# Optimization experiments

Hardware: AMD Instinct MI355X
Metric: run time of the kernel (lower is better)

Reference implementation:

```python
import jax, jax.numpy as jnp
import numpy as np

X, Y, F, B = 128, 128, 256, 2048
SIGMA = 2.0
LR = 0.5


def setup_inputs() -> dict:
    key = jax.random.key(0)
    k1, k2 = jax.random.split(key)
    data = jax.random.normal(k1, (B, F), dtype=jnp.float32)
    # weights init per module: 2*randn - 1, then L2-normalized along features
    w = 2.0 * jax.random.normal(k2, (X, Y, F), dtype=jnp.float32) - 1.0
    w = w / jnp.linalg.norm(w, axis=-1, keepdims=True)
    return {"data": data, "weights": w}


def reference(data, weights):
    # --- BMU search: euclidean cdist from each sample to every neuron ---
    wf = weights.reshape(X * Y, F)  # [N, F]
    d2 = (
        jnp.sum(data * data, axis=-1)[:, None]
        + jnp.sum(wf * wf, axis=-1)[None, :]
        - 2.0 * data @ wf.T
    )  # [B, N]
    dist = jnp.sqrt(jnp.maximum(d2, 0.0))
    idx = jnp.argmin(dist, axis=1)  # [B]
    bmu_x = idx // Y  # row coord
    bmu_y = idx % Y   # col coord

    # --- Gaussian neighborhood on the rectangular grid, one per sample ---
    xs = jnp.arange(X, dtype=jnp.float32)
    ys = jnp.arange(Y, dtype=jnp.float32)
    dx2 = (xs[None, :] - bmu_x[:, None].astype(jnp.float32)) ** 2  # [B, X]
    dy2 = (ys[None, :] - bmu_y[:, None].astype(jnp.float32)) ** 2  # [B, Y]
    nb = jnp.exp(-(dx2[:, :, None] + dy2[:, None, :]) / (2.0 * SIGMA * SIGMA))  # [B, X, Y]

    # --- Batch weight update: mean_b lr * nb_b * (data_b - W) ---
    # Avoid materializing the [B, X, Y, F] update tensor; same math via contraction.
    weighted_data = jnp.einsum("bxy,bf->xyf", nb, data)  # sum_b nb*data
    nb_sum = jnp.sum(nb, axis=0)  # [X, Y]
    new_weights = weights + (LR / B) * (weighted_data - nb_sum[..., None] * weights)
    return new_weights
```

## Files before the change

### kernel.cpp

```cpp
#include <hip/hip_runtime.h>
#include <hip/hip_fp16.h>

#define XD 128
#define YD 128
#define FD 256
#define BD 2048
#define ND (XD*YD)
#define LRB 2.44140625e-4f
#define RAD 14
#define MAXS 512

typedef _Float16 f16x8 __attribute__((ext_vector_type(8)));
typedef _Float16 f16x4 __attribute__((ext_vector_type(4)));
typedef float    f32x4 __attribute__((ext_vector_type(4)));

#define GLOAD_LDS16(g, l) \
  __builtin_amdgcn_global_load_lds((const __attribute__((address_space(1))) void*)(g), \
                                   (__attribute__((address_space(3))) void*)(l), 16, 0, 0)

__global__ __launch_bounds__(256) void init_kernel(unsigned long long* __restrict__ bmu_best) {
  int i = blockIdx.x * 256 + threadIdx.x;
  if (i < BD) bmu_best[i] = ~0ull;
}

__global__ __launch_bounds__(256) void rownorm2_kernel(const float* __restrict__ rows,
                                                       float* __restrict__ out) {
  int n = blockIdx.x * 4 + (threadIdx.x >> 6);
  int lane = threadIdx.x & 63;
  float4 v = *reinterpret_cast<const float4*>(rows + (size_t)n * FD + lane * 4);
  float s = v.x * v.x + v.y * v.y + v.z * v.z + v.w * v.w;
#pragma unroll
  for (int m = 32; m; m >>= 1) s += __shfl_xor(s, m);
  if (lane == 0) out[n] = s;
}

__global__ __launch_bounds__(256) void split_kernel(const float* __restrict__ src,
                                                    _Float16* __restrict__ hi,
                                                    _Float16* __restrict__ lo, int n4) {
  int i = blockIdx.x * 256 + threadIdx.x;
  if (i >= n4) return;
  float4 v = reinterpret_cast<const float4*>(src)[i];
  f16x4 h, l;
  h[0] = (_Float16)v.x; l[0] = (_Float16)((v.x - (float)h[0]) * 2048.0f);
  h[1] = (_Float16)v.y; l[1] = (_Float16)((v.y - (float)h[1]) * 2048.0f);
  h[2] = (_Float16)v.z; l[2] = (_Float16)((v.z - (float)h[2]) * 2048.0f);
  h[3] = (_Float16)v.w; l[3] = (_Float16)((v.w - (float)h[3]) * 2048.0f);
  reinterpret_cast<f16x4*>(hi)[i] = h;
  reinterpret_cast<f16x4*>(lo)[i] = l;
}

__device__ __forceinline__ f16x8 readfrag(const char* base, int r, int g) {
  int off = (r * 64 + 8 * g) ^ (((r >> 1) & 3) << 4);
  f16x4 a = *reinterpret_cast<const f16x4*>(base + off);
  f16x4 b = *reinterpret_cast<const f16x4*>(base + (off ^ 32));
  return __builtin_shufflevector(a, b, 0, 1, 2, 3, 4, 5, 6, 7);
}

__global__ __launch_bounds__(256, 2) void bmu_mfma_kernel(
    const _Float16* __restrict__ dh, const _Float16* __restrict__ dl,
    const _Float16* __restrict__ wh, const _Float16* __restrict__ wl,
    const float* __restrict__ wn2, const float* __restrict__ dn2,
    unsigned long long* __restrict__ bmu_best) {
  __shared__ char lds[32768];
  const int tid = threadIdx.x;
  const int lane = tid & 63;
  const int wid = tid >> 6;
  const int b0 = blockIdx.x * 128;
  const int n0 = blockIdx.y * 128;
  const int m0w = (wid >> 1) * 64;
  const int n0w = (wid & 1) * 64;
  const int lrow = lane & 15, lg = lane >> 4;

  f32x4 acch[4][4];
  f32x4 accx[4][4];
#pragma unroll
  for (int a = 0; a < 4; a++)
#pragma unroll
    for (int b = 0; b < 4; b++) { acch[a][b] = (f32x4)0.0f; accx[a][b] = (f32x4)0.0f; }

  const char* gbase =
      (wid == 0) ? (const char*)(dh + (size_t)b0 * FD) :
      (wid == 1) ? (const char*)(dl + (size_t)b0 * FD) :
      (wid == 2) ? (const char*)(wh + (size_t)n0 * FD) :
                   (const char*)(wl + (size_t)n0 * FD);
  char* lbase = (char*)lds + wid * 8192;

  const char* ldsAh = (const char*)lds;
  const char* ldsAl = (const char*)lds + 8192;
  const char* ldsBh = (const char*)lds + 16384;
  const char* ldsBl = (const char*)lds + 24576;

  for (int ks = 0; ks < 8; ks++) {
    __syncthreads();
#pragma unroll
    for (int c = 0; c < 8; c++) {
      int row = c * 16 + (lane >> 2);
      int wb = ((lane & 3) * 16) ^ (((row >> 1) & 3) << 4);
      const char* g = gbase + (size_t)row * 512 + ks * 64 + wb;
      GLOAD_LDS16(g, lbase + c * 1024);
    }
    __syncthreads();

    f16x8 ah[4], al[4];
#pragma unroll
    for (int mt = 0; mt < 4; mt++) {
      int r = m0w + mt * 16 + lrow;
      ah[mt] = readfrag(ldsAh, r, lg);
      al[mt] = readfrag(ldsAl, r, lg);
    }
#pragma unroll
    for (int nt = 0; nt < 4; nt++) {
      int r = n0w + nt * 16 + lrow;
      f16x8 bh = readfrag(ldsBh, r, lg);
      f16x8 bl = readfrag(ldsBl, r, lg);
#pragma unroll
      for (int mt = 0; mt < 4; mt++) {
        acch[mt][nt] = __builtin_amdgcn_mfma_f32_16x16x32_f16(ah[mt], bh, acch[mt][nt], 0, 0, 0);
        accx[mt][nt] = __builtin_amdgcn_mfma_f32_16x16x32_f16(ah[mt], bl, accx[mt][nt], 0, 0, 0);
        accx[mt][nt] = __builtin_amdgcn_mfma_f32_16x16x32_f16(al[mt], bh, accx[mt][nt], 0, 0, 0);
      }
    }
  }

#pragma unroll
  for (int mt = 0; mt < 4; mt++) {
    float d2s[4];
#pragma unroll
    for (int reg = 0; reg < 4; reg++)
      d2s[reg] = dn2[b0 + m0w + mt * 16 + lg * 4 + reg];
    unsigned long long bst[4] = {~0ull, ~0ull, ~0ull, ~0ull};
#pragma unroll
    for (int nt = 0; nt < 4; nt++) {
      int n = n0 + n0w + nt * 16 + lrow;
      float w2 = wn2[n];
#pragma unroll
      for (int reg = 0; reg < 4; reg++) {
        float dot = fmaf(accx[mt][nt][reg], 4.8828125e-4f, acch[mt][nt][reg]);
        float t1 = __fadd_rn(d2s[reg], w2);
        float d2v = __fsub_rn(t1, __fmul_rn(2.0f, dot));
        float dist = sqrtf(fmaxf(d2v, 0.0f));
        unsigned long long p = ((unsigned long long)__float_as_uint(dist) << 32) | (unsigned)n;
        bst[reg] = (p < bst[reg]) ? p : bst[reg];
      }
    }
#pragma unroll
    for (int m = 8; m; m >>= 1)
#pragma unroll
      for (int reg = 0; reg < 4; reg++) {
        unsigned long long o = __shfl_xor(bst[reg], m);
        bst[reg] = (o < bst[reg]) ? o : bst[reg];
      }
    if (lrow == 0)
#pragma unroll
      for (int reg = 0; reg < 4; reg++)
        atomicMin(&bmu_best[b0 + m0w + mt * 16 + lg * 4 + reg], bst[reg]);
  }
}

__global__ __launch_bounds__(256) void bmu_kernel(const float* __restrict__ data,
                                                  const float* __restrict__ w,
                                                  const float* __restrict__ wn2,
                                                  const float* __restrict__ dn2,
                                                  unsigned long long* __restrict__ bmu_best) {
  __shared__ float As[128][36];
  __shared__ float Bs[32][132];
  const int tid = threadIdx.x;
  const int b0 = blockIdx.x * 128;
  const int n0 = blockIdx.y * 128;
  const int g = tid >> 4;
  const int c = tid & 15;

  float acc[8][8] = {};

  for (int f0 = 0; f0 < FD; f0 += 32) {
    __syncthreads();
#pragma unroll
    for (int i = 0; i < 4; i++) {
      int idx = i * 256 + tid;
      int r = idx >> 3, c4 = (idx & 7) * 4;
      float4 v = *reinterpret_cast<const float4*>(data + (size_t)(b0 + r) * FD + f0 + c4);
      *reinterpret_cast<float4*>(&As[r][c4]) = v;
    }
#pragma unroll
    for (int i = 0; i < 4; i++) {
      int idx = i * 256 + tid;
      int r = idx >> 3, c4 = (idx & 7) * 4;
      float4 v = *reinterpret_cast<const float4*>(w + (size_t)(n0 + r) * FD + f0 + c4);
      Bs[c4 + 0][r] = v.x; Bs[c4 + 1][r] = v.y; Bs[c4 + 2][r] = v.z; Bs[c4 + 3][r] = v.w;
    }
    __syncthreads();
#pragma unroll
    for (int k0 = 0; k0 < 32; k0 += 4) {
      float4 a4[8];
#pragma unroll
      for (int i = 0; i < 8; i++)
        a4[i] = *reinterpret_cast<const float4*>(&As[g + 16 * i][k0]);
#pragma unroll
      for (int kk = 0; kk < 4; kk++) {
        float4 bl = *reinterpret_cast<const float4*>(&Bs[k0 + kk][c * 4]);
        float4 bh = *reinterpret_cast<const float4*>(&Bs[k0 + kk][c * 4 + 64]);
#pragma unroll
        for (int i = 0; i < 8; i++) {
          float a = (kk == 0) ? a4[i].x : (kk == 1) ? a4[i].y : (kk == 2) ? a4[i].z : a4[i].w;
          acc[i][0] = fmaf(a, bl.x, acc[i][0]);
          acc[i][1] = fmaf(a, bl.y, acc[i][1]);
          acc[i][2] = fmaf(a, bl.z, acc[i][2]);
          acc[i][3] = fmaf(a, bl.w, acc[i][3]);
          acc[i][4] = fmaf(a, bh.x, acc[i][4]);
          acc[i][5] = fmaf(a, bh.y, acc[i][5]);
          acc[i][6] = fmaf(a, bh.z, acc[i][6]);
          acc[i][7] = fmaf(a, bh.w, acc[i][7]);
        }
      }
    }
  }
  float w2[8];
#pragma unroll
  for (int j = 0; j < 8; j++) {
    int nl = (j < 4) ? (c * 4 + j) : (64 + c * 4 + (j - 4));
    w2[j] = wn2[n0 + nl];
  }
  unsigned long long best[8];
#pragma unroll
  for (int i = 0; i < 8; i++) {
    float dn2s = dn2[b0 + g + 16 * i];
    best[i] = ~0ull;
#pragma unroll
    for (int j = 0; j < 8; j++) {
      int nl = (j < 4) ? (c * 4 + j) : (64 + c * 4 + (j - 4));
      float t1 = __fadd_rn(dn2s, w2[j]);
      float d2v = __fsub_rn(t1, __fmul_rn(2.0f, acc[i][j]));
      float dist = sqrtf(fmaxf(d2v, 0.0f));
      unsigned long long p = ((unsigned long long)__float_as_uint(dist) << 32) | (unsigned)(n0 + nl);
      best[i] = (p < best[i]) ? p : best[i];
    }
  }
#pragma unroll
  for (int m = 8; m; m >>= 1)
#pragma unroll
    for (int i = 0; i < 8; i++) {
      unsigned long long o = __shfl_xor(best[i], m);
      best[i] = (o < best[i]) ? o : best[i];
    }
  if (c == 0)
#pragma unroll
    for (int i = 0; i < 8; i++)
      atomicMin(&bmu_best[b0 + g + 16 * i], best[i]);
}

__global__ __launch_bounds__(256) void update_kernel(const float* __restrict__ data,
                                                     const float* __restrict__ w,
                                                     const unsigned long long* __restrict__ bmu_best,
                                                     float* __restrict__ out) {
  __shared__ float axl[MAXS][4];
  __shared__ float ayl[MAXS][4];
  __shared__ int idxl[MAXS];
  __shared__ int cnt;
  __shared__ float red[16][17];
  __shared__ float nbsum_s[16];

  const int tid = threadIdx.x;
  const int tx0 = (blockIdx.x >> 5) * 4;
  const int ty0 = (blockIdx.x & 31) * 4;

  float acc[16] = {};
  float nbp = 0.f;
  const int myn = tid >> 4, q = tid & 15;
  const int mxi = myn >> 2, myi = myn & 3;

  for (int s0 = 0; s0 < BD; s0 += MAXS) {
    if (tid == 0) cnt = 0;
    __syncthreads();
#pragma unroll
    for (int i = 0; i < MAXS / 256; i++) {
      int s = s0 + i * 256 + tid;
      int bidx = (int)(bmu_best[s] & 0xFFFFFFFFull);
      int bx = bidx >> 7, by = bidx & 127;
      if (bx >= tx0 - RAD && bx <= tx0 + 3 + RAD &&
          by >= ty0 - RAD && by <= ty0 + 3 + RAD) {
        int pos = atomicAdd(&cnt, 1);
        idxl[pos] = s;
#pragma unroll
        for (int j = 0; j < 4; j++) {
          float dx = (float)(bx - (tx0 + j));
          float dy = (float)(by - (ty0 + j));
          axl[pos][j] = __expf(-dx * dx * 0.125f);
          ayl[pos][j] = __expf(-dy * dy * 0.125f);
        }
      }
    }
    __syncthreads();
    int cn = cnt;
    for (int s = 0; s < cn; s++) {
      float d = data[(size_t)idxl[s] * FD + tid];
#pragma unroll
      for (int xi = 0; xi < 4; xi++) {
        float t = axl[s][xi] * d;
#pragma unroll
        for (int yi = 0; yi < 4; yi++)
          acc[xi * 4 + yi] = fmaf(t, ayl[s][yi], acc[xi * 4 + yi]);
      }
    }
    for (int s = q; s < cn; s += 16) nbp += axl[s][mxi] * ayl[s][myi];
    __syncthreads();
  }

  red[myn][q] = nbp;
  __syncthreads();
  if (tid < 16) {
    float t = 0.f;
#pragma unroll
    for (int k = 0; k < 16; k++) t += red[tid][k];
    nbsum_s[tid] = t;
  }
  __syncthreads();

#pragma unroll
  for (int i = 0; i < 16; i++) {
    int n = (tx0 + (i >> 2)) * YD + (ty0 + (i & 3));
    size_t gi = (size_t)n * FD + tid;
    float wv = w[gi];
    out[gi] = fmaf(LRB, acc[i] - nbsum_s[i] * wv, wv);
  }
}

extern "C" void kernel_launch(void* const* d_in, const int* in_sizes, int n_in,
                              void* d_out, int out_size, void* d_ws, size_t ws_size,
                              hipStream_t stream) {
  const float* data = (const float*)d_in[0];
  const float* w = (const float*)d_in[1];
  float* out = (float*)d_out;

  char* ws = (char*)d_ws;
  float* wn2 = (float*)ws;
  float* dn2 = (float*)(ws + 65536);
  unsigned long long* bmu_best = (unsigned long long*)(ws + 73728);
  _Float16* dh = (_Float16*)(ws + 90112);
  _Float16* dl = (_Float16*)(ws + 1138688);
  _Float16* wh = (_Float16*)(ws + 2187264);
  _Float16* wl = (_Float16*)(ws + 10575872);
  const size_t WS_NEED = 18964480;

  init_kernel<<<(BD + 255) / 256, 256, 0, stream>>>(bmu_best);
  rownorm2_kernel<<<ND / 4, 256, 0, stream>>>(w, wn2);
  rownorm2_kernel<<<BD / 4, 256, 0, stream>>>(data, dn2);

  if (ws_size >= WS_NEED) {
    split_kernel<<<(BD * FD / 4 + 255) / 256, 256, 0, stream>>>(data, dh, dl, BD * FD / 4);
    split_kernel<<<(ND * FD / 4 + 255) / 256, 256, 0, stream>>>(w, wh, wl, ND * FD / 4);
    bmu_mfma_kernel<<<dim3(BD / 128, ND / 128), 256, 0, stream>>>(dh, dl, wh, wl, wn2, dn2, bmu_best);
  } else {
    bmu_kernel<<<dim3(BD / 128, ND / 128), 256, 0, stream>>>(data, w, wn2, dn2, bmu_best);
  }

  update_kernel<<<XD / 4 * (YD / 4), 256, 0, stream>>>(data, w, bmu_best, out);
}
```

Measured before the change: 201.6 us.

## Fuse prep kernels and double-buffer LDS staging in MFMA BMU kernel

Merges the init, row-norm and fp16 hi/lo split kernels into one prep kernel that writes the split operands already permuted and swizzled, so the GEMM can fetch each fragment with a single 16-byte LDS read. The BMU MFMA kernel now double-buffers its LDS tiles (64 KB), issuing the global-to-LDS loads for the next K slice while the current one computes, and drops one barrier per iteration. This targets launch overhead, the repeated reads of the inputs by the separate prep kernels, and the exposed load latency in the GEMM. The larger LDS footprint may lower occupancy below the two blocks per CU requested by the launch bounds.

```diff
diff --git a/kernel.cpp b/kernel.cpp
--- a/kernel.cpp
+++ b/kernel.cpp
@@ -18,42 +18,54 @@
   __builtin_amdgcn_global_load_lds((const __attribute__((address_space(1))) void*)(g), \
                                    (__attribute__((address_space(3))) void*)(l), 16, 0, 0)
 
-__global__ __launch_bounds__(256) void init_kernel(unsigned long long* __restrict__ bmu_best) {
-  int i = blockIdx.x * 256 + threadIdx.x;
-  if (i < BD) bmu_best[i] = ~0ull;
-}
-
-__global__ __launch_bounds__(256) void rownorm2_kernel(const float* __restrict__ rows,
-                                                       float* __restrict__ out) {
-  int n = blockIdx.x * 4 + (threadIdx.x >> 6);
-  int lane = threadIdx.x & 63;
-  float4 v = *reinterpret_cast<const float4*>(rows + (size_t)n * FD + lane * 4);
+__device__ __forceinline__ int swz(int row) { return ((row >> 1) & 3) << 4; }
+
+__global__ __launch_bounds__(256) void prep_kernel(
+    const float* __restrict__ data, const float* __restrict__ w,
+    _Float16* __restrict__ dh, _Float16* __restrict__ dl,
+    _Float16* __restrict__ wh, _Float16* __restrict__ wl,
+    float* __restrict__ dn2, float* __restrict__ wn2,
+    unsigned long long* __restrict__ bmu_best) {
+  const int tid = threadIdx.x;
+  const int bid = blockIdx.x;
+  if (bid < 8) bmu_best[bid * 256 + tid] = ~0ull;
+
+  const float* src; _Float16 *hi, *lo; float* nrm; int row;
+  if (bid < BD / 4) { src = data; hi = dh; lo = dl; nrm = dn2; row = bid * 4 + (tid >> 6); }
+  else { src = w; hi = wh; lo = wl; nrm = wn2; row = (bid - BD / 4) * 4 + (tid >> 6); }
+  const int lane = tid & 63;
+
+  float4 v = *reinterpret_cast<const float4*>(src + (size_t)row * FD + lane * 4);
   float s = v.x * v.x + v.y * v.y + v.z * v.z + v.w * v.w;
 #pragma unroll
   for (int m = 32; m; m >>= 1) s += __shfl_xor(s, m);
-  if (lane == 0) out[n] = s;
-}
-
-__global__ __launch_bounds__(256) void split_kernel(const float* __restrict__ src,
-                                                    _Float16* __restrict__ hi,
-                                                    _Float16* __restrict__ lo, int n4) {
-  int i = blockIdx.x * 256 + threadIdx.x;
-  if (i >= n4) return;
-  float4 v = reinterpret_cast<const float4*>(src)[i];
+  if (lane == 0) nrm[row] = s;
+
   f16x4 h, l;
   h[0] = (_Float16)v.x; l[0] = (_Float16)((v.x - (float)h[0]) * 2048.0f);
   h[1] = (_Float16)v.y; l[1] = (_Float16)((v.y - (float)h[1]) * 2048.0f);
   h[2] = (_Float16)v.z; l[2] = (_Float16)((v.z - (float)h[2]) * 2048.0f);
   h[3] = (_Float16)v.w; l[3] = (_Float16)((v.w - (float)h[3]) * 2048.0f);
-  reinterpret_cast<f16x4*>(hi)[i] = h;
-  reinterpret_cast<f16x4*>(lo)[i] = l;
-}
-
-__device__ __forceinline__ f16x8 readfrag(const char* base, int r, int g) {
-  int off = (r * 64 + 8 * g) ^ (((r >> 1) & 3) << 4);
-  f16x4 a = *reinterpret_cast<const f16x4*>(base + off);
-  f16x4 b = *reinterpret_cast<const f16x4*>(base + (off ^ 32));
-  return __builtin_shufflevector(a, b, 0, 1, 2, 3, 4, 5, 6, 7);
+
+  const int q = lane & 7, kb = lane >> 3;
+  const int slot = (q < 4) ? (q * 16) : ((q - 4) * 16 + 8);
+  const int off = kb * 64 + (slot ^ swz(row));
+  *reinterpret_cast<f16x4*>((char*)hi + (size_t)row * 512 + off) = h;
+  *reinterpret_cast<f16x4*>((char*)lo + (size_t)row * 512 + off) = l;
+}
+
+__device__ __forceinline__ f16x8 readfrag(const char* base, int r, int lg) {
+  int off = (r * 64 + lg * 16) ^ swz(r);
+  return *reinterpret_cast<const f16x8*>(base + off);
+}
+
+__device__ __forceinline__ void stage8(const char* gbase, char* lb, int ks, int lane) {
+#pragma unroll
+  for (int c = 0; c < 8; c++) {
+    int row = c * 16 + (lane >> 2);
+    const char* g = gbase + (size_t)row * 512 + (size_t)ks * 64 + (lane & 3) * 16;
+    GLOAD_LDS16(g, lb + c * 1024);
+  }
 }
 
 __global__ __launch_bounds__(256, 2) void bmu_mfma_kernel(
@@ -61,7 +73,7 @@
     const _Float16* __restrict__ wh, const _Float16* __restrict__ wl,
     const float* __restrict__ wn2, const float* __restrict__ dn2,
     unsigned long long* __restrict__ bmu_best) {
-  __shared__ char lds[32768];
+  __shared__ char lds[65536];
   const int tid = threadIdx.x;
   const int lane = tid & 63;
   const int wid = tid >> 6;
@@ -83,23 +95,18 @@
       (wid == 1) ? (const char*)(dl + (size_t)b0 * FD) :
       (wid == 2) ? (const char*)(wh + (size_t)n0 * FD) :
                    (const char*)(wl + (size_t)n0 * FD);
-  char* lbase = (char*)lds + wid * 8192;
-
-  const char* ldsAh = (const char*)lds;
-  const char* ldsAl = (const char*)lds + 8192;
-  const char* ldsBh = (const char*)lds + 16384;
-  const char* ldsBl = (const char*)lds + 24576;
+
+  stage8(gbase, (char*)lds + wid * 8192, 0, lane);
+  __syncthreads();
 
   for (int ks = 0; ks < 8; ks++) {
-    __syncthreads();
-#pragma unroll
-    for (int c = 0; c < 8; c++) {
-      int row = c * 16 + (lane >> 2);
-      int wb = ((lane & 3) * 16) ^ (((row >> 1) & 3) << 4);
-      const char* g = gbase + (size_t)row * 512 + ks * 64 + wb;
-      GLOAD_LDS16(g, lbase + c * 1024);
-    }
-    __syncthreads();
+    const int cur = ks & 1;
+    if (ks < 7) stage8(gbase, (char*)lds + (cur ^ 1) * 32768 + wid * 8192, ks + 1, lane);
+
+    const char* ldsAh = (const char*)lds + cur * 32768;
+    const char* ldsAl = ldsAh + 8192;
+    const char* ldsBh = ldsAh + 16384;
+    const char* ldsBl = ldsAh + 24576;
 
     f16x8 ah[4], al[4];
 #pragma unroll
@@ -120,6 +127,7 @@
         accx[mt][nt] = __builtin_amdgcn_mfma_f32_16x16x32_f16(al[mt], bh, accx[mt][nt], 0, 0, 0);
       }
     }
+    __syncthreads();
   }
 
 #pragma unroll
@@ -155,6 +163,21 @@
       for (int reg = 0; reg < 4; reg++)
         atomicMin(&bmu_best[b0 + m0w + mt * 16 + lg * 4 + reg], bst[reg]);
   }
+}
+
+__global__ __launch_bounds__(256) void init_kernel(unsigned long long* __restrict__ bmu_best) {
+  int i = blockIdx.x * 256 + threadIdx.x;
+  if (i < BD) bmu_best[i] = ~0ull;
+}
+__global__ __launch_bounds__(256) void rownorm2_kernel(const float* __restrict__ rows,
+                                                       float* __restrict__ out) {
+  int n = blockIdx.x * 4 + (threadIdx.x >> 6);
+  int lane = threadIdx.x & 63;
+  float4 v = *reinterpret_cast<const float4*>(rows + (size_t)n * FD + lane * 4);
+  float s = v.x * v.x + v.y * v.y + v.z * v.z + v.w * v.w;
+#pragma unroll
+  for (int m = 32; m; m >>= 1) s += __shfl_xor(s, m);
+  if (lane == 0) out[n] = s;
 }
 
 __global__ __launch_bounds__(256) void bmu_kernel(const float* __restrict__ data,
@@ -169,9 +192,7 @@
   const int n0 = blockIdx.y * 128;
   const int g = tid >> 4;
   const int c = tid & 15;
-
   float acc[8][8] = {};
-
   for (int f0 = 0; f0 < FD; f0 += 32) {
     __syncthreads();
 #pragma unroll
@@ -341,15 +362,13 @@
   _Float16* wl = (_Float16*)(ws + 10575872);
   const size_t WS_NEED = 18964480;
 
-  init_kernel<<<(BD + 255) / 256, 256, 0, stream>>>(bmu_best);
-  rownorm2_kernel<<<ND / 4, 256, 0, stream>>>(w, wn2);
-  rownorm2_kernel<<<BD / 4, 256, 0, stream>>>(data, dn2);
-
   if (ws_size >= WS_NEED) {
-    split_kernel<<<(BD * FD / 4 + 255) / 256, 256, 0, stream>>>(data, dh, dl, BD * FD / 4);
-    split_kernel<<<(ND * FD / 4 + 255) / 256, 256, 0, stream>>>(w, wh, wl, ND * FD / 4);
+    prep_kernel<<<BD / 4 + ND / 4, 256, 0, stream>>>(data, w, dh, dl, wh, wl, dn2, wn2, bmu_best);
     bmu_mfma_kernel<<<dim3(BD / 128, ND / 128), 256, 0, stream>>>(dh, dl, wh, wl, wn2, dn2, bmu_best);
   } else {
+    init_kernel<<<(BD + 255) / 256, 256, 0, stream>>>(bmu_best);
+    rownorm2_kernel<<<ND / 4, 256, 0, stream>>>(w, wn2);
+    rownorm2_kernel<<<BD / 4, 256, 0, stream>>>(data, dn2);
     bmu_kernel<<<dim3(BD / 128, ND / 128), 256, 0, stream>>>(data, w, wn2, dn2, bmu_best);
   }
 
```

Result: faster. 184.0 us (-8.7%).
